# Kernel tuning notes

Measured on AMD Instinct MI355X. Metric: run time of the kernel, lower is better.

Reference implementation:

```python
import jax, jax.numpy as jnp
import numpy as np

HIDDEN = 512
NUM_HEAD = 8
HEAD_DIM = HIDDEN // NUM_HEAD


def setup_inputs() -> dict:
    key = jax.random.key(0)
    ks = jax.random.split(key, 12)
    B, S = 8, 1024
    inp = {
        "v": jax.random.normal(ks[0], (B, S, HIDDEN), dtype=jnp.float32),
        "k": jax.random.normal(ks[1], (B, S, HIDDEN), dtype=jnp.float32),
        "q": jax.random.normal(ks[2], (B, S, HIDDEN), dtype=jnp.float32),
        "mask": jnp.zeros((B, 1, 1, S), dtype=bool),
    }
    scale = 1.0 / np.sqrt(HIDDEN)
    inp["Wv"] = jax.random.normal(ks[3], (HIDDEN, HIDDEN), dtype=jnp.float32) * scale
    inp["bv"] = jax.random.normal(ks[4], (HIDDEN,), dtype=jnp.float32) * scale
    inp["Wk"] = jax.random.normal(ks[5], (HIDDEN, HIDDEN), dtype=jnp.float32) * scale
    inp["bk"] = jax.random.normal(ks[6], (HIDDEN,), dtype=jnp.float32) * scale
    inp["Wq"] = jax.random.normal(ks[7], (HIDDEN, HIDDEN), dtype=jnp.float32) * scale
    inp["bq"] = jax.random.normal(ks[8], (HIDDEN,), dtype=jnp.float32) * scale
    inp["Wm"] = jax.random.normal(ks[9], (HIDDEN, HIDDEN), dtype=jnp.float32) * scale
    inp["bm"] = jax.random.normal(ks[10], (HIDDEN,), dtype=jnp.float32) * scale
    return inp


def _split_heads(x):
    # [B, S, H*D] -> [B, H, S, D]
    B, S, _ = x.shape
    return x.reshape(B, S, NUM_HEAD, HEAD_DIM).transpose(0, 2, 1, 3)


def reference(v, k, q, mask, Wv, bv, Wk, bk, Wq, bq, Wm, bm):
    B, S, _ = q.shape
    # linear projections (torch Linear: x @ W.T + b)
    vh = _split_heads(v @ Wv.T + bv)
    kh = _split_heads(k @ Wk.T + bk)
    qh = _split_heads(q @ Wq.T + bq)
    scale = 1.0 / jnp.sqrt(jnp.asarray(HEAD_DIM, dtype=qh.dtype))
    scores = jnp.einsum('bhqd,bhkd->bhqk', qh, kh) * scale
    scores = jnp.where(mask, jnp.asarray(-10000.0, dtype=scores.dtype), scores)
    att_map = jax.nn.softmax(scores, axis=-1)
    atted = jnp.einsum('bhqk,bhkd->bhqd', att_map, vh)
    atted = atted.transpose(0, 2, 1, 3).reshape(B, S, HIDDEN)
    atted = atted @ Wm.T + bm
    return atted, att_map
```

## Files before the change

kernel.cpp:

```cpp
#include <hip/hip_runtime.h>
#include <cstddef>

#define SEQ 1024
#define HID 512
#define NH 8
#define HD 64

typedef __attribute__((ext_vector_type(8))) short bf16x8;
typedef __attribute__((ext_vector_type(4))) float f32x4;

__device__ inline unsigned short f2bf(float f) {
  unsigned u = __builtin_bit_cast(unsigned, f);
  return (unsigned short)((u + 0x7fffu + ((u >> 16) & 1u)) >> 16);
}

__global__ __launch_bounds__(256) void proj_qkv(
    const float* __restrict__ x0, const float* __restrict__ x1, const float* __restrict__ x2,
    const float* __restrict__ w0, const float* __restrict__ w1, const float* __restrict__ w2,
    const float* __restrict__ b0, const float* __restrict__ b1, const float* __restrict__ b2,
    unsigned short* __restrict__ o0, unsigned short* __restrict__ o1,
    unsigned short* __restrict__ o2) {
  __shared__ __align__(16) char smem[32768];
  short* As = (short*)smem;
  short* Bs = As + 128 * 64;
  short* Cs = (short*)smem;

  const int z = blockIdx.z;
  const float* X = z == 0 ? x0 : (z == 1 ? x1 : x2);
  const float* W = z == 0 ? w0 : (z == 1 ? w1 : w2);
  const float* bias = z == 0 ? b0 : (z == 1 ? b1 : b2);
  unsigned short* out = z == 0 ? o0 : (z == 1 ? o1 : o2);
  const float scale = z == 0 ? 0.125f : 1.0f;

  const int t = threadIdx.x;
  const int lane = t & 63, wid = t >> 6;
  const int lg = lane >> 4, lr = lane & 15;
  const int wm = (wid >> 1) * 64, wn = (wid & 1) * 64;
  const int m0 = blockIdx.y * 128, n0 = blockIdx.x * 128;

  f32x4 acc[4][4];
  const f32x4 zf = {0.f, 0.f, 0.f, 0.f};
#pragma unroll
  for (int mg = 0; mg < 4; ++mg)
#pragma unroll
    for (int ng = 0; ng < 4; ++ng) acc[mg][ng] = zf;

  for (int k0 = 0; k0 < 512; k0 += 64) {
    __syncthreads();
#pragma unroll
    for (int i = 0; i < 4; ++i) {
      const int gi = t + i * 256;
      const int r = gi >> 3, g = gi & 7;
      const int dst = r * 64 + ((g ^ (r & 7)) * 8);
      {
        const float* src = X + (size_t)(m0 + r) * 512 + k0 + g * 8;
        const float4 a = *reinterpret_cast<const float4*>(src);
        const float4 b2 = *reinterpret_cast<const float4*>(src + 4);
        union { bf16x8 v; unsigned short u[8]; } p;
        p.u[0] = f2bf(a.x);  p.u[1] = f2bf(a.y);  p.u[2] = f2bf(a.z);  p.u[3] = f2bf(a.w);
        p.u[4] = f2bf(b2.x); p.u[5] = f2bf(b2.y); p.u[6] = f2bf(b2.z); p.u[7] = f2bf(b2.w);
        *reinterpret_cast<bf16x8*>(As + dst) = p.v;
      }
      {
        const float* srcw = W + (size_t)(n0 + r) * 512 + k0 + g * 8;
        const float4 wa = *reinterpret_cast<const float4*>(srcw);
        const float4 wb = *reinterpret_cast<const float4*>(srcw + 4);
        union { bf16x8 v; unsigned short u[8]; } q;
        q.u[0] = f2bf(wa.x); q.u[1] = f2bf(wa.y); q.u[2] = f2bf(wa.z); q.u[3] = f2bf(wa.w);
        q.u[4] = f2bf(wb.x); q.u[5] = f2bf(wb.y); q.u[6] = f2bf(wb.z); q.u[7] = f2bf(wb.w);
        *reinterpret_cast<bf16x8*>(Bs + dst) = q.v;
      }
    }
    __syncthreads();

#pragma unroll
    for (int c = 0; c < 2; ++c) {
      bf16x8 af[4], bfr[4];
#pragma unroll
      for (int mg = 0; mg < 4; ++mg) {
        const int r = wm + mg * 16 + lr;
        af[mg] = *reinterpret_cast<const bf16x8*>(As + r * 64 + (((lg + 4 * c) ^ (r & 7)) * 8));
      }
#pragma unroll
      for (int ng = 0; ng < 4; ++ng) {
        const int r = wn + ng * 16 + lr;
        bfr[ng] = *reinterpret_cast<const bf16x8*>(Bs + r * 64 + (((lg + 4 * c) ^ (r & 7)) * 8));
      }
#pragma unroll
      for (int mg = 0; mg < 4; ++mg)
#pragma unroll
        for (int ng = 0; ng < 4; ++ng)
          acc[mg][ng] =
              __builtin_amdgcn_mfma_f32_16x16x32_bf16(af[mg], bfr[ng], acc[mg][ng], 0, 0, 0);
    }
  }

  float bv[4];
#pragma unroll
  for (int ng = 0; ng < 4; ++ng) bv[ng] = bias[n0 + wn + ng * 16 + lr];

  __syncthreads();

  if (z == 2) {
#pragma unroll
    for (int mg = 0; mg < 4; ++mg) {
#pragma unroll
      for (int reg = 0; reg < 4; ++reg) {
        const int mi = wm + mg * 16 + 4 * lg + reg;
#pragma unroll
        for (int ng = 0; ng < 4; ++ng) {
          const int ni = wn + ng * 16 + lr;
          Cs[ni * 128 + (((mi >> 3) ^ (ni & 15)) * 8) + (mi & 7)] =
              f2bf(acc[mg][ng][reg] + bv[ng]);
        }
      }
    }
  } else {
#pragma unroll
    for (int mg = 0; mg < 4; ++mg) {
#pragma unroll
      for (int reg = 0; reg < 4; ++reg) {
        const int mi = wm + mg * 16 + 4 * lg + reg;
#pragma unroll
        for (int ng = 0; ng < 4; ++ng) {
          const int ni = wn + ng * 16 + lr;
          Cs[mi * 128 + ni] = f2bf((acc[mg][ng][reg] + bv[ng]) * scale);
        }
      }
    }
  }
  __syncthreads();

  const int bb = m0 >> 10;
  const int s_base = m0 & 1023;
  if (z == 2) {
#pragma unroll
    for (int rr = 0; rr < 8; ++rr) {
      const int e = t + rr * 256;
      const int dr = e >> 4;
      const int gm = e & 15;
      const bf16x8 v8 =
          *reinterpret_cast<const bf16x8*>(Cs + dr * 128 + ((gm ^ (dr & 15)) * 8));
      const int h = (n0 + dr) >> 6, d = (n0 + dr) & 63;
      *reinterpret_cast<bf16x8*>(
          out + (((size_t)(bb * NH + h)) * HD + d) * SEQ + s_base + gm * 8) = v8;
    }
  } else {
#pragma unroll
    for (int rr = 0; rr < 8; ++rr) {
      const int e = t + rr * 256;
      const int mi = e >> 4;
      const int gc = e & 15;
      const bf16x8 v8 = *reinterpret_cast<const bf16x8*>(Cs + mi * 128 + gc * 8);
      const int n = n0 + gc * 8;
      const int h = n >> 6, d = n & 63;
      *reinterpret_cast<bf16x8*>(
          out + (((size_t)(bb * NH + h)) * SEQ + s_base + mi) * HD + d) = v8;
    }
  }
}

__global__ __launch_bounds__(256) void proj_out(const unsigned short* __restrict__ Xb,
                                                const float* __restrict__ W,
                                                const float* __restrict__ bias,
                                                float* __restrict__ outv) {
  __shared__ short As[128 * 64];
  __shared__ short Bs[128 * 64];

  const int t = threadIdx.x;
  const int lane = t & 63, wid = t >> 6;
  const int lg = lane >> 4, lr = lane & 15;
  const int wm = (wid >> 1) * 64, wn = (wid & 1) * 64;
  const int m0 = blockIdx.y * 128, n0 = blockIdx.x * 128;

  f32x4 acc[4][4];
  const f32x4 zf = {0.f, 0.f, 0.f, 0.f};
#pragma unroll
  for (int mg = 0; mg < 4; ++mg)
#pragma unroll
    for (int ng = 0; ng < 4; ++ng) acc[mg][ng] = zf;

  for (int k0 = 0; k0 < 512; k0 += 64) {
    __syncthreads();
#pragma unroll
    for (int i = 0; i < 4; ++i) {
      const int gi = t + i * 256;
      const int r = gi >> 3, g = gi & 7;
      const int dst = r * 64 + ((g ^ (r & 7)) * 8);
      *reinterpret_cast<bf16x8*>(As + dst) =
          *reinterpret_cast<const bf16x8*>(Xb + (size_t)(m0 + r) * 512 + k0 + g * 8);
      const float* srcw = W + (size_t)(n0 + r) * 512 + k0 + g * 8;
      const float4 wa = *reinterpret_cast<const float4*>(srcw);
      const float4 wb = *reinterpret_cast<const float4*>(srcw + 4);
      union { bf16x8 v; unsigned short u[8]; } q;
      q.u[0] = f2bf(wa.x); q.u[1] = f2bf(wa.y); q.u[2] = f2bf(wa.z); q.u[3] = f2bf(wa.w);
      q.u[4] = f2bf(wb.x); q.u[5] = f2bf(wb.y); q.u[6] = f2bf(wb.z); q.u[7] = f2bf(wb.w);
      *reinterpret_cast<bf16x8*>(Bs + dst) = q.v;
    }
    __syncthreads();

#pragma unroll
    for (int c = 0; c < 2; ++c) {
      bf16x8 af[4], bfr[4];
#pragma unroll
      for (int mg = 0; mg < 4; ++mg) {
        const int r = wm + mg * 16 + lr;
        af[mg] = *reinterpret_cast<const bf16x8*>(As + r * 64 + (((lg + 4 * c) ^ (r & 7)) * 8));
      }
#pragma unroll
      for (int ng = 0; ng < 4; ++ng) {
        const int r = wn + ng * 16 + lr;
        bfr[ng] = *reinterpret_cast<const bf16x8*>(Bs + r * 64 + (((lg + 4 * c) ^ (r & 7)) * 8));
      }
#pragma unroll
      for (int mg = 0; mg < 4; ++mg)
#pragma unroll
        for (int ng = 0; ng < 4; ++ng)
          acc[mg][ng] =
              __builtin_amdgcn_mfma_f32_16x16x32_bf16(af[mg], bfr[ng], acc[mg][ng], 0, 0, 0);
    }
  }

  float bv[4];
#pragma unroll
  for (int ng = 0; ng < 4; ++ng) bv[ng] = bias[n0 + wn + ng * 16 + lr];

#pragma unroll
  for (int mg = 0; mg < 4; ++mg) {
#pragma unroll
    for (int reg = 0; reg < 4; ++reg) {
      const int m = m0 + wm + mg * 16 + 4 * lg + reg;
#pragma unroll
      for (int ng = 0; ng < 4; ++ng) {
        const int n = n0 + wn + ng * 16 + lr;
        __builtin_nontemporal_store(acc[mg][ng][reg] + bv[ng], outv + (size_t)m * 512 + n);
      }
    }
  }
}

__global__ __launch_bounds__(256, 4) void attn_fused(const unsigned short* __restrict__ qh,
                                                     const unsigned short* __restrict__ kh,
                                                     const unsigned short* __restrict__ vhT,
                                                     const unsigned char* __restrict__ mask,
                                                     float* __restrict__ att_map,
                                                     unsigned short* __restrict__ atted) {
  __shared__ short Vt[64 * 128];
  __shared__ short Pw4[4][2048];
  __shared__ float maskf[1024];

  const int t = threadIdx.x;
  const int lane = t & 63, wid = t >> 6;
  const int lg = lane >> 4, lr = lane & 15;
  const int qt = blockIdx.x & 15;
  const int bh = blockIdx.x >> 4;
  const int b = bh >> 3, h = bh & 7;
  const int q0 = qt * 64 + wid * 16;

  const unsigned short* Qb = qh + ((size_t)bh * SEQ + q0) * HD;
  const unsigned short* Kb = kh + (size_t)bh * SEQ * HD;
  const unsigned short* Vb = vhT + (size_t)bh * HD * SEQ;
  const unsigned char* mrow = mask + (size_t)b * SEQ;

#pragma unroll
  for (int i = 0; i < 4; ++i) {
    const int idx = t + i * 256;
    maskf[idx] = mrow[idx] ? -10000.f : 0.f;
  }

  bf16x8 qf[2];
#pragma unroll
  for (int c = 0; c < 2; ++c)
    qf[c] = *reinterpret_cast<const bf16x8*>(Qb + (size_t)lr * HD + lg * 8 + 32 * c);

  const f32x4 zf = {0.f, 0.f, 0.f, 0.f};
  f32x4 oacc[4] = {zf, zf, zf, zf};
  float rs = 0.f;
  short* Pw = Pw4[wid];

  for (int kt = 0; kt < 8; ++kt) {
    __syncthreads();
#pragma unroll
    for (int i = 0; i < 4; ++i) {
      const int gi = t + i * 256;
      const int d = gi >> 4, g = gi & 15;
      const int slot = (g & 8) | ((g & 7) ^ (d & 7));
      *reinterpret_cast<bf16x8*>(Vt + d * 128 + slot * 8) =
          *reinterpret_cast<const bf16x8*>(Vb + (size_t)d * SEQ + kt * 128 + g * 8);
    }
    __syncthreads();

#pragma unroll
    for (int cg = 0; cg < 8; ++cg) {
      const int r = kt * 128 + cg * 16 + lr;
      f32x4 s = zf;
#pragma unroll
      for (int c = 0; c < 2; ++c) {
        const bf16x8 kf =
            *reinterpret_cast<const bf16x8*>(Kb + (size_t)r * HD + (lg + 4 * c) * 8);
        s = __builtin_amdgcn_mfma_f32_16x16x32_bf16(kf, qf[c], s, 0, 0, 0);
      }
      const float4 madd =
          *reinterpret_cast<const float4*>(maskf + kt * 128 + cg * 16 + 4 * lg);
      const float p0 = __expf(s[0] + madd.x);
      const float p1 = __expf(s[1] + madd.y);
      const float p2 = __expf(s[2] + madd.z);
      const float p3 = __expf(s[3] + madd.w);
      rs += (p0 + p1) + (p2 + p3);
      uint2 pr;
      pr.x = (unsigned)f2bf(p0) | ((unsigned)f2bf(p1) << 16);
      pr.y = (unsigned)f2bf(p2) | ((unsigned)f2bf(p3) << 16);
      const int gk = 2 * cg + (lg >> 1);
      *reinterpret_cast<uint2*>(Pw + lr * 128 + ((gk ^ (lr & 7)) * 8) + (lg & 1) * 4) = pr;
    }

#pragma unroll
    for (int c = 0; c < 4; ++c) {
      const bf16x8 pa =
          *reinterpret_cast<const bf16x8*>(Pw + lr * 128 + (((lg + 4 * c) ^ (lr & 7)) * 8));
#pragma unroll
      for (int ng = 0; ng < 4; ++ng) {
        const int d = ng * 16 + lr;
        const int gidx = 4 * c + lg;
        const int slot = (gidx & 8) | ((gidx & 7) ^ (d & 7));
        const bf16x8 vf = *reinterpret_cast<const bf16x8*>(Vt + d * 128 + slot * 8);
        oacc[ng] = __builtin_amdgcn_mfma_f32_16x16x32_bf16(pa, vf, oacc[ng], 0, 0, 0);
      }
    }
  }

  rs += __shfl_xor(rs, 16);
  rs += __shfl_xor(rs, 32);
  const float inv = 1.f / rs;

  {
    float invq[4];
#pragma unroll
    for (int reg = 0; reg < 4; ++reg) invq[reg] = __shfl(inv, 4 * lg + reg);
#pragma unroll
    for (int ng = 0; ng < 4; ++ng) {
#pragma unroll
      for (int reg = 0; reg < 4; ++reg) {
        const int q = q0 + 4 * lg + reg;
        const int d = ng * 16 + lr;
        atted[((size_t)b * SEQ + q) * HID + h * HD + d] = f2bf(oacc[ng][reg] * invq[reg]);
      }
    }
  }

  float* arow = att_map + ((size_t)bh * SEQ + q0 + lr) * SEQ + 4 * lg;

  bf16x8 kfA[4][2], kfB[4][2];
  auto LD = [&](bf16x8 (&kf)[4][2], int it) {
    const int kt = it >> 1, h4 = (it & 1) * 4;
#pragma unroll
    for (int j = 0; j < 4; ++j) {
      const int r = kt * 128 + (h4 + j) * 16 + lr;
#pragma unroll
      for (int c = 0; c < 2; ++c)
        kf[j][c] =
            *reinterpret_cast<const bf16x8*>(Kb + (size_t)r * HD + (lg + 4 * c) * 8);
    }
  };
  auto CS = [&](bf16x8 (&kf)[4][2], int it) {
    const int kt = it >> 1, h4 = (it & 1) * 4;
#pragma unroll
    for (int j = 0; j < 4; ++j) {
      f32x4 s = zf;
      s = __builtin_amdgcn_mfma_f32_16x16x32_bf16(kf[j][0], qf[0], s, 0, 0, 0);
      s = __builtin_amdgcn_mfma_f32_16x16x32_bf16(kf[j][1], qf[1], s, 0, 0, 0);
      const int kbase = kt * 128 + (h4 + j) * 16;
      const float4 madd = *reinterpret_cast<const float4*>(maskf + kbase + 4 * lg);
      f32x4 w;
      w.x = __expf(s[0] + madd.x) * inv;
      w.y = __expf(s[1] + madd.y) * inv;
      w.z = __expf(s[2] + madd.z) * inv;
      w.w = __expf(s[3] + madd.w) * inv;
      __builtin_nontemporal_store(w, reinterpret_cast<f32x4*>(arow + kbase));
    }
  };

  LD(kfA, 0);
#pragma unroll
  for (int ip = 0; ip < 8; ++ip) {
    LD(kfB, ip * 2 + 1);
    CS(kfA, ip * 2);
    if (ip * 2 + 2 < 16) LD(kfA, ip * 2 + 2);
    CS(kfB, ip * 2 + 1);
  }
}

extern "C" void kernel_launch(void* const* d_in, const int* in_sizes, int n_in,
                              void* d_out, int out_size, void* d_ws, size_t ws_size,
                              hipStream_t stream) {
  const float* v = (const float*)d_in[0];
  const float* k = (const float*)d_in[1];
  const float* q = (const float*)d_in[2];
  const unsigned char* mask = (const unsigned char*)d_in[3];
  const float* Wv = (const float*)d_in[4];
  const float* bv = (const float*)d_in[5];
  const float* Wk = (const float*)d_in[6];
  const float* bk = (const float*)d_in[7];
  const float* Wq = (const float*)d_in[8];
  const float* bq = (const float*)d_in[9];
  const float* Wm = (const float*)d_in[10];
  const float* bm = (const float*)d_in[11];

  float* out_atted = (float*)d_out;
  float* out_att = out_atted + (size_t)8 * SEQ * HID;

  const size_t TN = (size_t)8 * SEQ * HID;
  unsigned short* qh = (unsigned short*)d_ws;
  unsigned short* kh = qh + TN;
  unsigned short* vhT = kh + TN;
  unsigned short* aw = vhT + TN;

  proj_qkv<<<dim3(4, 64, 3), 256, 0, stream>>>(q, k, v, Wq, Wk, Wv, bq, bk, bv, qh, kh, vhT);

  attn_fused<<<dim3(1024), 256, 0, stream>>>(qh, kh, vhT, mask, out_att, aw);

  proj_out<<<dim3(4, 64), 256, 0, stream>>>(aw, Wm, bm, out_atted);
}
```

Before: 203.3 us.

## Split attention keys across wave pairs, drop V LDS staging, stage out-proj stores

The attention kernel now gives each query tile of 16 rows to a pair of waves. Each wave handles half of the keys, and the two partial outputs and row sums are combined through LDS. The grid doubles, occupancy is raised to 6 blocks per CU, and V is read directly from global memory instead of being staged in LDS with a block-wide sync. The mask is read as bytes instead of being precomputed into LDS. The output projection now stages results in LDS so it can write coalesced 16-byte rows. This trades extra global and L2 V traffic and a cross-wave reduction for fewer barriers and more parallelism.

New measurement: 250.2 us. +23.1%, slower.

```diff
diff --git a/kernel.cpp b/kernel.cpp
--- a/kernel.cpp
+++ b/kernel.cpp
@@ -164,8 +164,10 @@
                                                 const float* __restrict__ W,
                                                 const float* __restrict__ bias,
                                                 float* __restrict__ outv) {
-  __shared__ short As[128 * 64];
-  __shared__ short Bs[128 * 64];
+  __shared__ __align__(16) char smem[32768];
+  short* As = (short*)smem;
+  short* Bs = As + 128 * 64;
+  float* Cs = (float*)smem;
 
   const int t = threadIdx.x;
   const int lane = t & 63, wid = t >> 6;
@@ -225,49 +227,59 @@
 #pragma unroll
   for (int ng = 0; ng < 4; ++ng) bv[ng] = bias[n0 + wn + ng * 16 + lr];
 
-#pragma unroll
-  for (int mg = 0; mg < 4; ++mg) {
-#pragma unroll
-    for (int reg = 0; reg < 4; ++reg) {
-      const int m = m0 + wm + mg * 16 + 4 * lg + reg;
-#pragma unroll
-      for (int ng = 0; ng < 4; ++ng) {
-        const int n = n0 + wn + ng * 16 + lr;
-        __builtin_nontemporal_store(acc[mg][ng][reg] + bv[ng], outv + (size_t)m * 512 + n);
-      }
-    }
+  __syncthreads();
+
+#pragma unroll
+  for (int half = 0; half < 2; ++half) {
+    if ((wid >> 1) == half) {
+#pragma unroll
+      for (int mg = 0; mg < 4; ++mg) {
+#pragma unroll
+        for (int reg = 0; reg < 4; ++reg) {
+          const int row = mg * 16 + 4 * lg + reg;
+#pragma unroll
+          for (int ng = 0; ng < 4; ++ng)
+            Cs[row * 128 + wn + ng * 16 + lr] = acc[mg][ng][reg] + bv[ng];
+        }
+      }
+    }
+    __syncthreads();
+#pragma unroll
+    for (int rr = 0; rr < 8; ++rr) {
+      const int g = t + rr * 256;
+      const int row = g >> 5;
+      const int gc = g & 31;
+      const f32x4 w4 = *reinterpret_cast<const f32x4*>(Cs + row * 128 + gc * 4);
+      *reinterpret_cast<f32x4*>(outv + (size_t)(m0 + half * 64 + row) * 512 + n0 + gc * 4) = w4;
+    }
+    __syncthreads();
   }
 }
 
-__global__ __launch_bounds__(256, 4) void attn_fused(const unsigned short* __restrict__ qh,
+__global__ __launch_bounds__(256, 6) void attn_fused(const unsigned short* __restrict__ qh,
                                                      const unsigned short* __restrict__ kh,
                                                      const unsigned short* __restrict__ vhT,
                                                      const unsigned char* __restrict__ mask,
                                                      float* __restrict__ att_map,
                                                      unsigned short* __restrict__ atted) {
-  __shared__ short Vt[64 * 128];
   __shared__ short Pw4[4][2048];
-  __shared__ float maskf[1024];
+  __shared__ float rsbuf[4][16];
 
   const int t = threadIdx.x;
   const int lane = t & 63, wid = t >> 6;
   const int lg = lane >> 4, lr = lane & 15;
-  const int qt = blockIdx.x & 15;
-  const int bh = blockIdx.x >> 4;
+  const int pair = wid >> 1, w = wid & 1;
+  const int qt = blockIdx.x & 31;
+  const int bh = blockIdx.x >> 5;
   const int b = bh >> 3, h = bh & 7;
-  const int q0 = qt * 64 + wid * 16;
+  const int q0 = qt * 32 + pair * 16;
+  const int k0w = w * 512;
 
   const unsigned short* Qb = qh + ((size_t)bh * SEQ + q0) * HD;
   const unsigned short* Kb = kh + (size_t)bh * SEQ * HD;
   const unsigned short* Vb = vhT + (size_t)bh * HD * SEQ;
   const unsigned char* mrow = mask + (size_t)b * SEQ;
 
-#pragma unroll
-  for (int i = 0; i < 4; ++i) {
-    const int idx = t + i * 256;
-    maskf[idx] = mrow[idx] ? -10000.f : 0.f;
-  }
-
   bf16x8 qf[2];
 #pragma unroll
   for (int c = 0; c < 2; ++c)
@@ -278,21 +290,11 @@
   float rs = 0.f;
   short* Pw = Pw4[wid];
 
-  for (int kt = 0; kt < 8; ++kt) {
-    __syncthreads();
-#pragma unroll
-    for (int i = 0; i < 4; ++i) {
-      const int gi = t + i * 256;
-      const int d = gi >> 4, g = gi & 15;
-      const int slot = (g & 8) | ((g & 7) ^ (d & 7));
-      *reinterpret_cast<bf16x8*>(Vt + d * 128 + slot * 8) =
-          *reinterpret_cast<const bf16x8*>(Vb + (size_t)d * SEQ + kt * 128 + g * 8);
-    }
-    __syncthreads();
-
+  for (int kt = 0; kt < 4; ++kt) {
+    const int kb = k0w + kt * 128;
 #pragma unroll
     for (int cg = 0; cg < 8; ++cg) {
-      const int r = kt * 128 + cg * 16 + lr;
+      const int r = kb + cg * 16 + lr;
       f32x4 s = zf;
 #pragma unroll
       for (int c = 0; c < 2; ++c) {
@@ -300,12 +302,11 @@
             *reinterpret_cast<const bf16x8*>(Kb + (size_t)r * HD + (lg + 4 * c) * 8);
         s = __builtin_amdgcn_mfma_f32_16x16x32_bf16(kf, qf[c], s, 0, 0, 0);
       }
-      const float4 madd =
-          *reinterpret_cast<const float4*>(maskf + kt * 128 + cg * 16 + 4 * lg);
-      const float p0 = __expf(s[0] + madd.x);
-      const float p1 = __expf(s[1] + madd.y);
-      const float p2 = __expf(s[2] + madd.z);
-      const float p3 = __expf(s[3] + madd.w);
+      const uchar4 m4 = *reinterpret_cast<const uchar4*>(mrow + kb + cg * 16 + 4 * lg);
+      const float p0 = __expf(s[0] + (m4.x ? -10000.f : 0.f));
+      const float p1 = __expf(s[1] + (m4.y ? -10000.f : 0.f));
+      const float p2 = __expf(s[2] + (m4.z ? -10000.f : 0.f));
+      const float p3 = __expf(s[3] + (m4.w ? -10000.f : 0.f));
       rs += (p0 + p1) + (p2 + p3);
       uint2 pr;
       pr.x = (unsigned)f2bf(p0) | ((unsigned)f2bf(p1) << 16);
@@ -321,9 +322,8 @@
 #pragma unroll
       for (int ng = 0; ng < 4; ++ng) {
         const int d = ng * 16 + lr;
-        const int gidx = 4 * c + lg;
-        const int slot = (gidx & 8) | ((gidx & 7) ^ (d & 7));
-        const bf16x8 vf = *reinterpret_cast<const bf16x8*>(Vt + d * 128 + slot * 8);
+        const bf16x8 vf = *reinterpret_cast<const bf16x8*>(
+            Vb + (size_t)d * SEQ + kb + (4 * c + lg) * 8);
         oacc[ng] = __builtin_amdgcn_mfma_f32_16x16x32_bf16(pa, vf, oacc[ng], 0, 0, 0);
       }
     }
@@ -331,9 +331,21 @@
 
   rs += __shfl_xor(rs, 16);
   rs += __shfl_xor(rs, 32);
-  const float inv = 1.f / rs;
-
-  {
+  if (lane < 16) rsbuf[wid][lane] = rs;
+  if (w == 1) {
+    float* ob = (float*)Pw;
+#pragma unroll
+    for (int ng = 0; ng < 4; ++ng)
+#pragma unroll
+      for (int reg = 0; reg < 4; ++reg)
+        ob[(4 * lg + reg) * 64 + ng * 16 + lr] = oacc[ng][reg];
+  }
+  __syncthreads();
+
+  const float inv = 1.f / (rsbuf[pair * 2][lr] + rsbuf[pair * 2 + 1][lr]);
+
+  if (w == 0) {
+    const float* ob = (const float*)(Pw4[wid + 1]);
     float invq[4];
 #pragma unroll
     for (int reg = 0; reg < 4; ++reg) invq[reg] = __shfl(inv, 4 * lg + reg);
@@ -343,50 +355,53 @@
       for (int reg = 0; reg < 4; ++reg) {
         const int q = q0 + 4 * lg + reg;
         const int d = ng * 16 + lr;
-        atted[((size_t)b * SEQ + q) * HID + h * HD + d] = f2bf(oacc[ng][reg] * invq[reg]);
-      }
-    }
-  }
-
-  float* arow = att_map + ((size_t)bh * SEQ + q0 + lr) * SEQ + 4 * lg;
-
-  bf16x8 kfA[4][2], kfB[4][2];
-  auto LD = [&](bf16x8 (&kf)[4][2], int it) {
-    const int kt = it >> 1, h4 = (it & 1) * 4;
-#pragma unroll
-    for (int j = 0; j < 4; ++j) {
-      const int r = kt * 128 + (h4 + j) * 16 + lr;
+        const float o = oacc[ng][reg] + ob[(4 * lg + reg) * 64 + d];
+        atted[((size_t)b * SEQ + q) * HID + h * HD + d] = f2bf(o * invq[reg]);
+      }
+    }
+  }
+
+  float* arow = att_map + ((size_t)bh * SEQ + q0 + lr) * SEQ + k0w + 4 * lg;
+
+  bf16x8 kA[2][2], kB[2][2];
+  auto LD = [&](bf16x8 (&kf)[2][2], int it) {
+    const int kt = it >> 2, cgp = (it & 3) * 2;
+#pragma unroll
+    for (int j = 0; j < 2; ++j) {
+      const int r = k0w + kt * 128 + (cgp + j) * 16 + lr;
 #pragma unroll
       for (int c = 0; c < 2; ++c)
         kf[j][c] =
             *reinterpret_cast<const bf16x8*>(Kb + (size_t)r * HD + (lg + 4 * c) * 8);
     }
   };
-  auto CS = [&](bf16x8 (&kf)[4][2], int it) {
-    const int kt = it >> 1, h4 = (it & 1) * 4;
-#pragma unroll
-    for (int j = 0; j < 4; ++j) {
+  auto CS = [&](bf16x8 (&kf)[2][2], int it) {
+    const int kt = it >> 2, cgp = (it & 3) * 2;
+#pragma unroll
+    for (int j = 0; j < 2; ++j) {
+      const int cg = cgp + j;
       f32x4 s = zf;
       s = __builtin_amdgcn_mfma_f32_16x16x32_bf16(kf[j][0], qf[0], s, 0, 0, 0);
       s = __builtin_amdgcn_mfma_f32_16x16x32_bf16(kf[j][1], qf[1], s, 0, 0, 0);
-      const int kbase = kt * 128 + (h4 + j) * 16;
-      const float4 madd = *reinterpret_cast<const float4*>(maskf + kbase + 4 * lg);
-      f32x4 w;
-      w.x = __expf(s[0] + madd.x) * inv;
-      w.y = __expf(s[1] + madd.y) * inv;
-      w.z = __expf(s[2] + madd.z) * inv;
-      w.w = __expf(s[3] + madd.w) * inv;
-      __builtin_nontemporal_store(w, reinterpret_cast<f32x4*>(arow + kbase));
+      const uchar4 m4 =
+          *reinterpret_cast<const uchar4*>(mrow + k0w + kt * 128 + cg * 16 + 4 * lg);
+      f32x4 wv;
+      wv.x = __expf(s[0] + (m4.x ? -10000.f : 0.f)) * inv;
+      wv.y = __expf(s[1] + (m4.y ? -10000.f : 0.f)) * inv;
+      wv.z = __expf(s[2] + (m4.z ? -10000.f : 0.f)) * inv;
+      wv.w = __expf(s[3] + (m4.w ? -10000.f : 0.f)) * inv;
+      __builtin_nontemporal_store(
+          wv, reinterpret_cast<f32x4*>(arow + kt * 128 + cg * 16));
     }
   };
 
-  LD(kfA, 0);
+  LD(kA, 0);
 #pragma unroll
   for (int ip = 0; ip < 8; ++ip) {
-    LD(kfB, ip * 2 + 1);
-    CS(kfA, ip * 2);
-    if (ip * 2 + 2 < 16) LD(kfA, ip * 2 + 2);
-    CS(kfB, ip * 2 + 1);
+    LD(kB, ip * 2 + 1);
+    CS(kA, ip * 2);
+    if (ip * 2 + 2 < 16) LD(kA, ip * 2 + 2);
+    CS(kB, ip * 2 + 1);
   }
 }
 
@@ -417,7 +432,7 @@
 
   proj_qkv<<<dim3(4, 64, 3), 256, 0, stream>>>(q, k, v, Wq, Wk, Wv, bq, bk, bv, qh, kh, vhT);
 
-  attn_fused<<<dim3(1024), 256, 0, stream>>>(qh, kh, vhT, mask, out_att, aw);
+  attn_fused<<<dim3(2048), 256, 0, stream>>>(qh, kh, vhT, mask, out_att, aw);
 
   proj_out<<<dim3(4, 64), 256, 0, stream>>>(aw, Wm, bm, out_atted);
 }
```
